# Kernel tuning notes

Measured on AMD Instinct MI355X. Metric: run time of the kernel, lower is better.

Reference implementation:

```python
import jax, jax.numpy as jnp
import numpy as np


def setup_inputs() -> dict:
    key = jax.random.key(0)
    k0, k1, k2, k3, k4 = jax.random.split(key, 5)
    B, S, D, H = 64, 512, 512, 512
    scale = 1.0 / np.sqrt(H)
    inp = {
        "input_features": jax.random.normal(k0, (B, S, D), dtype=jnp.float32),
        # PyTorch GRU params, gate order (r, z, n)
        "W_ih": jax.random.uniform(k1, (3 * H, D), jnp.float32, -scale, scale),
        "W_hh": jax.random.uniform(k2, (3 * H, H), jnp.float32, -scale, scale),
        "b_ih": jax.random.uniform(k3, (3 * H,), jnp.float32, -scale, scale),
        "b_hh": jax.random.uniform(k4, (3 * H,), jnp.float32, -scale, scale),
    }
    return inp


def reference(input_features, W_ih, W_hh, b_ih, b_hh):
    """1-layer unidirectional GRU with residual connection (input_dim == hidden_dim,
    so self.linear is Identity). Returns (residual_output [B,S,H],
    stacked per-step hidden [1,B,S,H]) matching the torch module."""
    B, S, D = input_features.shape
    H = W_hh.shape[1]

    # Precompute input projections for all timesteps in one GEMM: [B,S,3H]
    x_proj = jnp.einsum("bsd,gd->bsg", input_features, W_ih) + b_ih
    x_proj_t = jnp.transpose(x_proj, (1, 0, 2))  # [S,B,3H]

    def step(h, xp):
        # xp: [B,3H], h: [B,H]
        gh = h @ W_hh.T + b_hh  # [B,3H]
        r = jax.nn.sigmoid(xp[:, :H] + gh[:, :H])
        z = jax.nn.sigmoid(xp[:, H:2 * H] + gh[:, H:2 * H])
        n = jnp.tanh(xp[:, 2 * H:] + r * gh[:, 2 * H:])
        h_new = (1.0 - z) * n + z * h
        return h_new, h_new

    h0 = jnp.zeros((B, H), dtype=input_features.dtype)
    _, hs = jax.lax.scan(step, h0, x_proj_t)  # hs: [S,B,H]
    outputs = jnp.transpose(hs, (1, 0, 2))  # [B,S,H] raw GRU outputs

    residual_output = input_features + outputs  # Identity residual (D == H)
    hidden_stacked = outputs[None]  # [1,B,S,H]: per-step hidden of the single layer
    return residual_output, hidden_stacked
```

## Files before the change

### kernel.cpp

```cpp
#include <hip/hip_runtime.h>

typedef unsigned short u16;
typedef unsigned int   u32;
typedef unsigned long long u64;
typedef __attribute__((ext_vector_type(4))) float f32x4;
typedef __attribute__((ext_vector_type(8))) short s16x8;
typedef __attribute__((ext_vector_type(4))) unsigned short u16x4;
typedef __attribute__((ext_vector_type(8))) unsigned short u16x8;

__device__ __forceinline__ float bf2f(u16 u) {
    u32 i = ((u32)u) << 16;
    return __builtin_bit_cast(float, i);
}
__device__ __forceinline__ u16 f2bf(float f) {
    u32 i = __builtin_bit_cast(u32, f);
    u32 lsb = (i >> 16) & 1u;
    i += 0x7fffu + lsb;
    return (u16)(i >> 16);
}

__global__ __launch_bounds__(256) void prep(const float* __restrict__ Wih,
                                            const float* __restrict__ Whh,
                                            u16* __restrict__ Wihb,
                                            u16* __restrict__ Wfrag) {
    int id = blockIdx.x * 256 + threadIdx.x;
    {
        const float* s = Wih + (size_t)id * 8;
        f32x4 x0 = *(const f32x4*)s;
        f32x4 x1 = *(const f32x4*)(s + 4);
        u16x8 o;
        for (int j = 0; j < 4; ++j) { o[j] = f2bf(x0[j]); o[4 + j] = f2bf(x1[j]); }
        *(u16x8*)(Wihb + (size_t)id * 8) = o;
    }
    {
        int lane = id & 63;
        int ks   = (id >> 6) & 15;
        int wnt  = id >> 10;
        int nt   = wnt % 3;
        int w    = wnt / 3;
        int row  = nt * 512 + w * 16 + (lane & 15);
        int k    = ks * 32 + (lane >> 4) * 8;
        const float* s = Whh + (size_t)row * 512 + k;
        f32x4 x0 = *(const f32x4*)s;
        f32x4 x1 = *(const f32x4*)(s + 4);
        u16x8 o;
        for (int j = 0; j < 4; ++j) { o[j] = f2bf(x0[j]); o[4 + j] = f2bf(x1[j]); }
        *(u16x8*)(Wfrag + (size_t)id * 8) = o;
    }
}

__global__ __launch_bounds__(256) void gemm_xproj(const float* __restrict__ inp,
                                                  const u16* __restrict__ Wihb,
                                                  const float* __restrict__ bih,
                                                  u16* __restrict__ xp) {
    __shared__ u16 lA[128 * 64];
    __shared__ u16 lB[128 * 64];
    const int bid = blockIdx.x;
    const int mtile = bid & 255;
    const int ntile = bid >> 8;
    const int tid = threadIdx.x;
    const int l = tid & 63;
    const int wid = tid >> 6;
    const int s0 = mtile * 2;
    const int n0 = ntile * 128;

    f32x4 acc[4][4];
    for (int a = 0; a < 4; ++a)
        for (int b = 0; b < 4; ++b) acc[a][b] = (f32x4){0.f, 0.f, 0.f, 0.f};

    for (int k0 = 0; k0 < 512; k0 += 64) {
        if (k0) __syncthreads();
        for (int i = 0; i < 4; ++i) {
            int boff = (wid * 4 + i) * 1024 + l * 16;
            int r = boff >> 7;
            int kb = boff & 127;
            const char* src = (const char*)Wihb + (size_t)(n0 + r) * 1024 + (size_t)k0 * 2 + kb;
            __builtin_amdgcn_global_load_lds(
                (const __attribute__((address_space(1))) u32*)src,
                (__attribute__((address_space(3))) u32*)((char*)lB + (wid * 4 + i) * 1024),
                16, 0, 0);
        }
        for (int i = 0; i < 4; ++i) {
            int c = i * 256 + tid;
            int r = c >> 3;
            int ck = c & 7;
            int b = r & 63;
            int sl = r >> 6;
            const float* src = inp + ((size_t)(b * 512 + s0 + sl) * 512 + k0 + ck * 8);
            f32x4 x0 = *(const f32x4*)src;
            f32x4 x1 = *(const f32x4*)(src + 4);
            u16x8 o;
            for (int j = 0; j < 4; ++j) { o[j] = f2bf(x0[j]); o[4 + j] = f2bf(x1[j]); }
            *(u16x8*)(&lA[r * 64 + ck * 8]) = o;
        }
        __syncthreads();
        for (int kk = 0; kk < 2; ++kk) {
            s16x8 af[4], bf[4];
            for (int am = 0; am < 4; ++am)
                af[am] = *(const s16x8*)(&lA[((wid >> 1) * 64 + am * 16 + (l & 15)) * 64 + kk * 32 + (l >> 4) * 8]);
            for (int bn = 0; bn < 4; ++bn)
                bf[bn] = *(const s16x8*)(&lB[((wid & 1) * 64 + bn * 16 + (l & 15)) * 64 + kk * 32 + (l >> 4) * 8]);
            for (int am = 0; am < 4; ++am)
                for (int bn = 0; bn < 4; ++bn)
                    acc[am][bn] = __builtin_amdgcn_mfma_f32_16x16x32_bf16(af[am], bf[bn], acc[am][bn], 0, 0, 0);
        }
    }
    for (int am = 0; am < 4; ++am) {
        for (int bn = 0; bn < 4; ++bn) {
            int m_base = mtile * 128 + (wid >> 1) * 64 + am * 16;
            int row0 = m_base + ((l >> 4) << 2);
            int s = row0 >> 6;
            int b0 = row0 & 63;
            int n = n0 + (wid & 1) * 64 + bn * 16 + (l & 15);
            int g = n >> 9;
            int col = n & 511;
            int ww = col >> 4;
            int mt2 = b0 >> 4;
            size_t el = ((((size_t)s * 32 + ww) * 4 + mt2) * 3 + g) * 256 + l * 4;
            float bias = bih[n];
            u16x4 o;
            for (int j = 0; j < 4; ++j) o[j] = f2bf(acc[am][bn][j] + bias);
            *(u16x4*)(xp + el) = o;
        }
    }
}

__global__ __launch_bounds__(256) void gru_scan(const u16* __restrict__ xp,
                                                const u16* __restrict__ Wfrag,
                                                const float* __restrict__ bhh,
                                                const float* __restrict__ inp,
                                                float* __restrict__ dout,
                                                u16* __restrict__ hbuf,
                                                int* __restrict__ cnt) {
    const int w = blockIdx.x;
    const int tid = threadIdx.x;
    const int l = tid & 63;
    const int mt = tid >> 6;
    float* out_res = dout;
    float* out_hid = dout + (size_t)64 * 512 * 512;

    __shared__ u16 wlds[3 * 16 * 64 * 8];
    const char* wsrc = (const char*)(Wfrag + (size_t)w * 24576);
    for (int i = 0; i < 12; ++i) {
        int doff = (mt * 12 + i) * 1024;
        __builtin_amdgcn_global_load_lds(
            (const __attribute__((address_space(1))) u32*)(wsrc + doff + l * 16),
            (__attribute__((address_space(3))) u32*)((char*)wlds + doff),
            16, 0, 0);
    }
    const float bh0 = bhh[0 * 512 + w * 16 + (l & 15)];
    const float bh1 = bhh[1 * 512 + w * 16 + (l & 15)];
    const float bh2 = bhh[2 * 512 + w * 16 + (l & 15)];
    float hold[4] = {0.f, 0.f, 0.f, 0.f};
    const int bb = mt * 16 + ((l >> 4) << 2);
    const int c = w * 16 + (l & 15);
    __syncthreads();

    for (int t = 0; t < 512; ++t) {
        const u16* xpp = xp + ((((size_t)t * 32 + w) * 4 + mt) * 3) * 256 + l * 4;
        u16x4 xv0 = *(const u16x4*)(xpp);
        u16x4 xv1 = *(const u16x4*)(xpp + 256);
        u16x4 xv2 = *(const u16x4*)(xpp + 512);
        float inv[4];
        for (int j = 0; j < 4; ++j)
            inv[j] = inp[((size_t)(bb + j) * 512 + t) * 512 + c];

        if (t > 0) {
            __syncthreads();
            if (tid == 0) {
                __hip_atomic_fetch_add(&cnt[t - 1], 1, __ATOMIC_RELAXED, __HIP_MEMORY_SCOPE_AGENT);
                while (__hip_atomic_load(&cnt[t - 1], __ATOMIC_RELAXED, __HIP_MEMORY_SCOPE_AGENT) < 32) {}
            }
            __syncthreads();
        }

        const u16* hr = hbuf + (size_t)(t & 1) * 32768;
        u16* hw = hbuf + (size_t)((t + 1) & 1) * 32768;

        const u64* hbase = (const u64*)(hr + (size_t)(mt * 16 + (l & 15)) * 512 + ((l >> 4) << 3));
        s16x8 af[16];
        for (int kk = 0; kk < 16; ++kk) {
            u64 lo = __hip_atomic_load(hbase + kk * 8, __ATOMIC_RELAXED, __HIP_MEMORY_SCOPE_AGENT);
            u64 hi = __hip_atomic_load(hbase + kk * 8 + 1, __ATOMIC_RELAXED, __HIP_MEMORY_SCOPE_AGENT);
            union { u64 q[2]; s16x8 v; } u;
            u.q[0] = lo; u.q[1] = hi;
            af[kk] = u.v;
        }

        f32x4 acc0 = (f32x4){0.f, 0.f, 0.f, 0.f};
        f32x4 acc1 = (f32x4){0.f, 0.f, 0.f, 0.f};
        f32x4 acc2 = (f32x4){0.f, 0.f, 0.f, 0.f};
        for (int kk = 0; kk < 16; ++kk) {
            s16x8 b0 = *(const s16x8*)(&wlds[(0 * 16 + kk) * 512 + l * 8]);
            s16x8 b1 = *(const s16x8*)(&wlds[(1 * 16 + kk) * 512 + l * 8]);
            s16x8 b2 = *(const s16x8*)(&wlds[(2 * 16 + kk) * 512 + l * 8]);
            acc0 = __builtin_amdgcn_mfma_f32_16x16x32_bf16(af[kk], b0, acc0, 0, 0, 0);
            acc1 = __builtin_amdgcn_mfma_f32_16x16x32_bf16(af[kk], b1, acc1, 0, 0, 0);
            acc2 = __builtin_amdgcn_mfma_f32_16x16x32_bf16(af[kk], b2, acc2, 0, 0, 0);
        }

        float hn[4];
        for (int j = 0; j < 4; ++j) {
            float xr = bf2f(xv0[j]), xz = bf2f(xv1[j]), xn = bf2f(xv2[j]);
            float rr = 1.f / (1.f + __expf(-(xr + acc0[j] + bh0)));
            float zz = 1.f / (1.f + __expf(-(xz + acc1[j] + bh1)));
            float nx = xn + rr * (acc2[j] + bh2);
            float e2 = __expf(-2.f * nx);
            float nn = (1.f - e2) / (1.f + e2);
            float h = (1.f - zz) * nn + zz * hold[j];
            hold[j] = h;
            hn[j] = h;
        }
        for (int j = 0; j < 4; ++j) {
            __hip_atomic_store(hw + (size_t)(bb + j) * 512 + c, f2bf(hn[j]),
                               __ATOMIC_RELAXED, __HIP_MEMORY_SCOPE_AGENT);
            size_t oi = ((size_t)(bb + j) * 512 + t) * 512 + c;
            out_hid[oi] = hn[j];
            out_res[oi] = inv[j] + hn[j];
        }
    }
}

extern "C" void kernel_launch(void* const* d_in, const int* in_sizes, int n_in,
                              void* d_out, int out_size, void* d_ws, size_t ws_size,
                              hipStream_t stream) {
    const float* inp = (const float*)d_in[0];
    const float* Wih = (const float*)d_in[1];
    const float* Whh = (const float*)d_in[2];
    const float* bih = (const float*)d_in[3];
    const float* bhh = (const float*)d_in[4];
    float* out = (float*)d_out;

    char* ws = (char*)d_ws;
    int* cnt   = (int*)ws;
    u16* hbuf  = (u16*)(ws + 4096);
    u16* Wfrag = (u16*)(ws + 135168);
    u16* Wihb  = (u16*)(ws + 1708032);
    u16* xp    = (u16*)(ws + 3280896);

    hipMemsetAsync(ws, 0, 4096 + 65536, stream);
    hipLaunchKernelGGL(prep, dim3(384), dim3(256), 0, stream, Wih, Whh, Wihb, Wfrag);
    hipLaunchKernelGGL(gemm_xproj, dim3(3072), dim3(256), 0, stream, inp, Wihb, bih, xp);
    hipLaunchKernelGGL(gru_scan, dim3(32), dim3(256), 0, stream, xp, Wfrag, bhh, inp, out, hbuf, cnt);
}
```

Before: 2.858 ms.

## Replace block barrier sync with per-wave counters and register-resident recurrent weights

The GRU scan now keeps the W_hh fragments in registers instead of LDS and drops the per-step __syncthreads plus tid-0 spin. Each wave publishes its hidden slice through an LDS transpose as a coalesced 8-byte cache-bypassing store and bumps a counter, then spins until all 128 waves have arrived. Inputs for the next step are prefetched before the spin, and the h reads use sc0 sc1 vector loads instead of 64-bit atomics. The aim is shorter latency on the serial critical path, at the cost of heavy register pressure and 128 spinning waves hitting one counter.

```diff
diff --git a/kernel.cpp b/kernel.cpp
--- a/kernel.cpp
+++ b/kernel.cpp
@@ -17,6 +17,13 @@
     u32 lsb = (i >> 16) & 1u;
     i += 0x7fffu + lsb;
     return (u16)(i >> 16);
+}
+
+__device__ __forceinline__ void ld_cc16(s16x8& r, const u16* p) {
+    asm volatile("global_load_dwordx4 %0, %1, off sc0 sc1" : "=v"(r) : "v"(p));
+}
+__device__ __forceinline__ void st_cc8(u16* p, u64 v) {
+    asm volatile("global_store_dwordx2 %0, %1, off sc0 sc1" :: "v"(p), "v"(v) : "memory");
 }
 
 __global__ __launch_bounds__(256) void prep(const float* __restrict__ Wih,
@@ -125,13 +132,13 @@
     }
 }
 
-__global__ __launch_bounds__(256) void gru_scan(const u16* __restrict__ xp,
-                                                const u16* __restrict__ Wfrag,
-                                                const float* __restrict__ bhh,
-                                                const float* __restrict__ inp,
-                                                float* __restrict__ dout,
-                                                u16* __restrict__ hbuf,
-                                                int* __restrict__ cnt) {
+__global__ __launch_bounds__(256, 1) void gru_scan(const u16* __restrict__ xp,
+                                                   const u16* __restrict__ Wfrag,
+                                                   const float* __restrict__ bhh,
+                                                   const float* __restrict__ inp,
+                                                   float* __restrict__ dout,
+                                                   u16* __restrict__ hbuf,
+                                                   int* __restrict__ cnt) {
     const int w = blockIdx.x;
     const int tid = threadIdx.x;
     const int l = tid & 63;
@@ -139,67 +146,52 @@
     float* out_res = dout;
     float* out_hid = dout + (size_t)64 * 512 * 512;
 
-    __shared__ u16 wlds[3 * 16 * 64 * 8];
-    const char* wsrc = (const char*)(Wfrag + (size_t)w * 24576);
-    for (int i = 0; i < 12; ++i) {
-        int doff = (mt * 12 + i) * 1024;
-        __builtin_amdgcn_global_load_lds(
-            (const __attribute__((address_space(1))) u32*)(wsrc + doff + l * 16),
-            (__attribute__((address_space(3))) u32*)((char*)wlds + doff),
-            16, 0, 0);
-    }
+    __shared__ u16 tlds[4][16][20];
+
+    const u16* wsrc = Wfrag + (size_t)w * 24576;
+    s16x8 wreg[3][16];
+#pragma unroll
+    for (int g = 0; g < 3; ++g)
+#pragma unroll
+        for (int kk = 0; kk < 16; ++kk)
+            wreg[g][kk] = *(const s16x8*)(wsrc + (size_t)(g * 16 + kk) * 512 + l * 8);
+
     const float bh0 = bhh[0 * 512 + w * 16 + (l & 15)];
     const float bh1 = bhh[1 * 512 + w * 16 + (l & 15)];
     const float bh2 = bhh[2 * 512 + w * 16 + (l & 15)];
     float hold[4] = {0.f, 0.f, 0.f, 0.f};
     const int bb = mt * 16 + ((l >> 4) << 2);
     const int c = w * 16 + (l & 15);
-    __syncthreads();
+
+    s16x8 af[16];
+#pragma unroll
+    for (int kk = 0; kk < 16; ++kk) af[kk] = (s16x8){0, 0, 0, 0, 0, 0, 0, 0};
+
+    const u16* xpp = xp + ((((size_t)0 * 32 + w) * 4 + mt) * 3) * 256 + l * 4;
+    u16x4 xv0 = *(const u16x4*)(xpp);
+    u16x4 xv1 = *(const u16x4*)(xpp + 256);
+    u16x4 xv2 = *(const u16x4*)(xpp + 512);
+    float inv[4];
+#pragma unroll
+    for (int j = 0; j < 4; ++j)
+        inv[j] = inp[((size_t)(bb + j) * 512 + 0) * 512 + c];
 
     for (int t = 0; t < 512; ++t) {
-        const u16* xpp = xp + ((((size_t)t * 32 + w) * 4 + mt) * 3) * 256 + l * 4;
-        u16x4 xv0 = *(const u16x4*)(xpp);
-        u16x4 xv1 = *(const u16x4*)(xpp + 256);
-        u16x4 xv2 = *(const u16x4*)(xpp + 512);
-        float inv[4];
-        for (int j = 0; j < 4; ++j)
-            inv[j] = inp[((size_t)(bb + j) * 512 + t) * 512 + c];
-
-        if (t > 0) {
-            __syncthreads();
-            if (tid == 0) {
-                __hip_atomic_fetch_add(&cnt[t - 1], 1, __ATOMIC_RELAXED, __HIP_MEMORY_SCOPE_AGENT);
-                while (__hip_atomic_load(&cnt[t - 1], __ATOMIC_RELAXED, __HIP_MEMORY_SCOPE_AGENT) < 32) {}
-            }
-            __syncthreads();
-        }
-
-        const u16* hr = hbuf + (size_t)(t & 1) * 32768;
-        u16* hw = hbuf + (size_t)((t + 1) & 1) * 32768;
-
-        const u64* hbase = (const u64*)(hr + (size_t)(mt * 16 + (l & 15)) * 512 + ((l >> 4) << 3));
-        s16x8 af[16];
-        for (int kk = 0; kk < 16; ++kk) {
-            u64 lo = __hip_atomic_load(hbase + kk * 8, __ATOMIC_RELAXED, __HIP_MEMORY_SCOPE_AGENT);
-            u64 hi = __hip_atomic_load(hbase + kk * 8 + 1, __ATOMIC_RELAXED, __HIP_MEMORY_SCOPE_AGENT);
-            union { u64 q[2]; s16x8 v; } u;
-            u.q[0] = lo; u.q[1] = hi;
-            af[kk] = u.v;
-        }
+        asm volatile("s_waitcnt vmcnt(0)" ::: "memory");
+        __builtin_amdgcn_sched_barrier(0);
 
         f32x4 acc0 = (f32x4){0.f, 0.f, 0.f, 0.f};
         f32x4 acc1 = (f32x4){0.f, 0.f, 0.f, 0.f};
         f32x4 acc2 = (f32x4){0.f, 0.f, 0.f, 0.f};
+#pragma unroll
         for (int kk = 0; kk < 16; ++kk) {
-            s16x8 b0 = *(const s16x8*)(&wlds[(0 * 16 + kk) * 512 + l * 8]);
-            s16x8 b1 = *(const s16x8*)(&wlds[(1 * 16 + kk) * 512 + l * 8]);
-            s16x8 b2 = *(const s16x8*)(&wlds[(2 * 16 + kk) * 512 + l * 8]);
-            acc0 = __builtin_amdgcn_mfma_f32_16x16x32_bf16(af[kk], b0, acc0, 0, 0, 0);
-            acc1 = __builtin_amdgcn_mfma_f32_16x16x32_bf16(af[kk], b1, acc1, 0, 0, 0);
-            acc2 = __builtin_amdgcn_mfma_f32_16x16x32_bf16(af[kk], b2, acc2, 0, 0, 0);
+            acc0 = __builtin_amdgcn_mfma_f32_16x16x32_bf16(af[kk], wreg[0][kk], acc0, 0, 0, 0);
+            acc1 = __builtin_amdgcn_mfma_f32_16x16x32_bf16(af[kk], wreg[1][kk], acc1, 0, 0, 0);
+            acc2 = __builtin_amdgcn_mfma_f32_16x16x32_bf16(af[kk], wreg[2][kk], acc2, 0, 0, 0);
         }
 
         float hn[4];
+#pragma unroll
         for (int j = 0; j < 4; ++j) {
             float xr = bf2f(xv0[j]), xz = bf2f(xv1[j]), xn = bf2f(xv2[j]);
             float rr = 1.f / (1.f + __expf(-(xr + acc0[j] + bh0)));
@@ -211,12 +203,43 @@
             hold[j] = h;
             hn[j] = h;
         }
+
+        if (t < 511) {
+#pragma unroll
+            for (int j = 0; j < 4; ++j)
+                tlds[mt][((l >> 4) << 2) + j][l & 15] = f2bf(hn[j]);
+            u64 hv = *(const u64*)(&tlds[mt][l >> 2][(l & 3) * 4]);
+            u16* hw = hbuf + (size_t)((t + 1) & 1) * 32768;
+            st_cc8(hw + (size_t)(mt * 16 + (l >> 2)) * 512 + w * 16 + (l & 3) * 4, hv);
+            asm volatile("s_waitcnt vmcnt(0)" ::: "memory");
+            if (l == 0)
+                __hip_atomic_fetch_add(&cnt[t], 1, __ATOMIC_RELAXED, __HIP_MEMORY_SCOPE_AGENT);
+        }
+
+#pragma unroll
         for (int j = 0; j < 4; ++j) {
-            __hip_atomic_store(hw + (size_t)(bb + j) * 512 + c, f2bf(hn[j]),
-                               __ATOMIC_RELAXED, __HIP_MEMORY_SCOPE_AGENT);
             size_t oi = ((size_t)(bb + j) * 512 + t) * 512 + c;
             out_hid[oi] = hn[j];
             out_res[oi] = inv[j] + hn[j];
+        }
+
+        if (t < 511) {
+            const u16* xq = xp + ((((size_t)(t + 1) * 32 + w) * 4 + mt) * 3) * 256 + l * 4;
+            xv0 = *(const u16x4*)(xq);
+            xv1 = *(const u16x4*)(xq + 256);
+            xv2 = *(const u16x4*)(xq + 512);
+#pragma unroll
+            for (int j = 0; j < 4; ++j)
+                inv[j] = inp[((size_t)(bb + j) * 512 + t + 1) * 512 + c];
+
+            while (__hip_atomic_load(&cnt[t], __ATOMIC_RELAXED, __HIP_MEMORY_SCOPE_AGENT) < 128) {}
+            __builtin_amdgcn_sched_barrier(0);
+
+            const u16* hr = hbuf + (size_t)((t + 1) & 1) * 32768;
+            const u16* hb = hr + (size_t)(mt * 16 + (l & 15)) * 512 + ((l >> 4) << 3);
+#pragma unroll
+            for (int kk = 0; kk < 16; ++kk)
+                ld_cc16(af[kk], hb + kk * 32);
         }
     }
 }
@@ -238,7 +261,7 @@
     u16* Wihb  = (u16*)(ws + 1708032);
     u16* xp    = (u16*)(ws + 3280896);
 
-    hipMemsetAsync(ws, 0, 4096 + 65536, stream);
+    hipMemsetAsync(ws, 0, 4096, stream);
     hipLaunchKernelGGL(prep, dim3(384), dim3(256), 0, stream, Wih, Whh, Wihb, Wfrag);
     hipLaunchKernelGGL(gemm_xproj, dim3(3072), dim3(256), 0, stream, inp, Wihb, bih, xp);
     hipLaunchKernelGGL(gru_scan, dim3(32), dim3(256), 0, stream, xp, Wfrag, bhh, inp, out, hbuf, cnt);
```

Result: slower. 3.254 ms (+13.9%).
